# Kernel tuning notes

Hardware: AMD Instinct MI355X
Metric: run time of the kernel (lower is better)

The kernel has to match this reference:

```python
import jax, jax.numpy as jnp
import numpy as np

NUM_HEADS = 16
MAX_LEN = 2048


def setup_inputs() -> dict:
    key = jax.random.key(0)
    ks = jax.random.split(key, 10)
    L, B, C = 2048, 2, 1024
    s = 0.02
    return {
        "x": jax.random.normal(ks[0], (L, B, C), dtype=jnp.float32),
        "Wq": jax.random.normal(ks[1], (C, C), dtype=jnp.float32) * s,
        "bq": jnp.zeros((C,), dtype=jnp.float32),
        "Wk": jax.random.normal(ks[2], (C, C), dtype=jnp.float32) * s,
        "bk": jnp.zeros((C,), dtype=jnp.float32),
        "Wv": jax.random.normal(ks[3], (C, C), dtype=jnp.float32) * s,
        "bv": jnp.zeros((C,), dtype=jnp.float32),
        "Wo": jax.random.normal(ks[4], (C, C), dtype=jnp.float32) * s,
        "bo": jnp.zeros((C,), dtype=jnp.float32),
        "rel": jax.random.normal(ks[5], (2 * MAX_LEN - 1,), dtype=jnp.float32) * s,
    }


def reference(x, Wq, bq, Wk, bk, Wv, bv, Wo, bo, rel):
    L, B, C = x.shape
    H = NUM_HEADS
    hd = C // H
    scale = hd ** (-0.5)
    xb = jnp.transpose(x, (1, 0, 2))  # (B, L, C)

    def heads(y):  # (B, L, C) -> (B, H, L, hd)
        return jnp.transpose(y.reshape(B, L, H, hd), (0, 2, 1, 3))

    Q = heads(xb @ Wq + bq)
    K = heads(xb @ Wk + bk)
    V = heads(xb @ Wv + bv)

    scores = jnp.einsum("bhqd,bhkd->bhqk", Q, K)  # (B, H, L, L)
    # relative-position bias gather: offset = k - q + max_len - 1
    idx = jnp.arange(L)[None, :] - jnp.arange(L)[:, None] + (MAX_LEN - 1)
    R = rel[idx]  # (L, L)
    scores = (scores + R[None, None, :, :]) * scale
    w = jax.nn.softmax(scores, axis=-1)
    attn = jnp.einsum("bhqk,bhkd->bhqd", w, V)  # (B, H, L, hd)
    attn = jnp.transpose(attn, (0, 2, 1, 3)).reshape(B, L, C)
    attn = jnp.transpose(attn, (1, 0, 2))  # (L, B, C)
    return attn @ Wo + bo
```

## Files before the change

kernel.cpp:

```cpp
#include <hip/hip_runtime.h>

#define L_SEQ 2048
#define BATCH 2
#define CDIM  1024
#define NH    16
#define HD    64

typedef __attribute__((ext_vector_type(8))) short short8;
typedef __attribute__((ext_vector_type(4))) float floatx4;

#define QSCALE 0.18033688011112042f

__device__ __forceinline__ unsigned short f2bf(float f){
  unsigned int u = __builtin_bit_cast(unsigned int, f);
  u += 0x7fffu + ((u >> 16) & 1u);
  return (unsigned short)(u >> 16);
}

__device__ __forceinline__ void gload_lds16(const void* g, void* l){
  typedef __attribute__((address_space(1))) void gv_t;
  typedef __attribute__((address_space(3))) void sv_t;
  __builtin_amdgcn_global_load_lds((gv_t*)(void*)g, (sv_t*)l, 16, 0, 0);
}

__global__ void __launch_bounds__(256) prep_x(const float* __restrict__ x,
                                              unsigned short* __restrict__ xb){
  int idx = blockIdx.x * 256 + threadIdx.x;
  int c4 = idx & 255;
  int lb = idx >> 8;
  int b  = lb & (BATCH - 1);
  int l  = lb >> 1;
  float4 v = ((const float4*)x)[idx];
  ushort4 s;
  s.x = f2bf(v.x); s.y = f2bf(v.y); s.z = f2bf(v.z); s.w = f2bf(v.w);
  *(ushort4*)&xb[(size_t)(b*L_SEQ + l)*CDIM + c4*4] = s;
}

__global__ void __launch_bounds__(256) prep_w(const float* __restrict__ Wq,
    const float* __restrict__ Wk, const float* __restrict__ Wv,
    const float* __restrict__ Wo, unsigned short* __restrict__ Wqkvt,
    unsigned short* __restrict__ Wot){
  __shared__ float tile[32][33];
  int z = blockIdx.z;
  const float* W = (z==0)?Wq:(z==1)?Wk:(z==2)?Wv:Wo;
  unsigned short* dst = (z==3) ? Wot : (Wqkvt + (size_t)z*CDIM*CDIM);
  int tx = threadIdx.x & 31, ty = threadIdx.x >> 5;
  int X = blockIdx.x*32, Y = blockIdx.y*32;
  #pragma unroll
  for (int i=0;i<4;i++)
    tile[ty + i*8][tx] = W[(size_t)(Y + ty + i*8)*CDIM + X + tx];
  __syncthreads();
  #pragma unroll
  for (int i=0;i<4;i++)
    dst[(size_t)(X + ty + i*8)*CDIM + Y + tx] = f2bf(tile[tx][ty + i*8]);
}

template<int MODE>
__global__ void __launch_bounds__(256) gemm_bt(
    const unsigned short* __restrict__ A,
    const unsigned short* __restrict__ Bt,
    int Kdim,
    const float* __restrict__ b0, const float* __restrict__ b1,
    const float* __restrict__ b2,
    unsigned short* __restrict__ qo, unsigned short* __restrict__ ko,
    unsigned short* __restrict__ vo, float* __restrict__ out)
{
  __shared__ unsigned short Asm[128*32];
  __shared__ unsigned short Bsm[128*32];
  const int t    = threadIdx.x;
  const int lane = t & 63;
  const int wave = t >> 6;
  const int wr = wave >> 1, wc = wave & 1;
  const int g = lane >> 4, lr = lane & 15;
  const int rowA0 = blockIdx.x * 128;
  const int rowB0 = blockIdx.y * 128;

  floatx4 acc[4][4] = {};

  const int r_st = t >> 2;
  const int k_st = (t & 3) * 8;

  for (int k0 = 0; k0 < Kdim; k0 += 32) {
    const unsigned short* ga = A  + (size_t)(rowA0 + r_st) * Kdim + k0 + k_st;
    const unsigned short* gb = Bt + (size_t)(rowB0 + r_st) * Kdim + k0 + k_st;
    gload_lds16(ga,                   &Asm[t*8]);
    gload_lds16(ga + (size_t)64*Kdim, &Asm[2048 + t*8]);
    gload_lds16(gb,                   &Bsm[t*8]);
    gload_lds16(gb + (size_t)64*Kdim, &Bsm[2048 + t*8]);
    __syncthreads();
    short8 af[4], bfr[4];
    #pragma unroll
    for (int mi=0;mi<4;mi++)
      af[mi] = *(const short8*)&Asm[(wr*64 + mi*16 + lr)*32 + g*8];
    #pragma unroll
    for (int ni=0;ni<4;ni++)
      bfr[ni] = *(const short8*)&Bsm[(wc*64 + ni*16 + lr)*32 + g*8];
    #pragma unroll
    for (int mi=0;mi<4;mi++)
      #pragma unroll
      for (int ni=0;ni<4;ni++)
        acc[mi][ni] = __builtin_amdgcn_mfma_f32_16x16x32_bf16(af[mi], bfr[ni], acc[mi][ni], 0, 0, 0);
    __syncthreads();
  }

  #pragma unroll
  for (int mi=0;mi<4;mi++){
    const int rb = rowA0 + wr*64 + mi*16 + g*4;
    #pragma unroll
    for (int ni=0;ni<4;ni++){
      const int col = rowB0 + wc*64 + ni*16 + lr;
      if (MODE == 0) {
        const int sec = col >> 10;
        const int nl  = col & 1023;
        const int h = nl >> 6, d = nl & 63;
        const float* bp = (sec==0) ? b0 : (sec==1) ? b1 : b2;
        const float bias = bp[nl];
        #pragma unroll
        for (int r=0;r<4;r++){
          const int row = rb + r;
          const int b = row >> 11, l = row & 2047;
          float v = acc[mi][ni][r] + bias;
          if (sec == 0) v *= QSCALE;
          const unsigned short hv = f2bf(v);
          const size_t bh = (size_t)(b*NH + h);
          if (sec == 0)      qo[(bh*L_SEQ + l)*HD + d] = hv;
          else if (sec == 1) ko[(bh*L_SEQ + l)*HD + d] = hv;
          else               vo[(bh*HD + d)*L_SEQ + l] = hv;
        }
      } else {
        const float bias = b0[col];
        #pragma unroll
        for (int r=0;r<4;r++){
          const int row = rb + r;
          const int b = row >> 11, l = row & 2047;
          out[((size_t)l*BATCH + b)*CDIM + col] = acc[mi][ni][r] + bias;
        }
      }
    }
  }
}

__global__ void __launch_bounds__(256) attn_kernel(
    const unsigned short* __restrict__ Qb, const unsigned short* __restrict__ Kb,
    const unsigned short* __restrict__ Vt, const float* __restrict__ rel,
    unsigned short* __restrict__ Ab)
{
  __shared__ unsigned short Ks[2][64*64];
  __shared__ unsigned short Vs[2][64*64];
  __shared__ unsigned int Pl[4*16*32];
  const int bh = blockIdx.x;
  const int qb = blockIdx.y;
  const int t = threadIdx.x, lane = t & 63, wave = t >> 6;
  const int g = lane >> 4, lr = lane & 15;

  const unsigned short* Qp = Qb + (size_t)bh * (L_SEQ*HD);
  const unsigned short* Kp = Kb + (size_t)bh * (L_SEQ*HD);
  const unsigned short* Vp = Vt + (size_t)bh * (HD*L_SEQ);

  const int q0 = qb*64 + wave*16;
  const short8 qf0 = *(const short8*)&Qp[(size_t)(q0 + lr)*HD + g*8];
  const short8 qf1 = *(const short8*)&Qp[(size_t)(q0 + lr)*HD + 32 + g*8];

  const float* relp = rel + (2047 - q0 - lr + g*4);

  unsigned int* pw = Pl + wave*512 + lr*32;
  const int swz = lr & 7;

  const int srow = t >> 3;
  const int sxor = (t & 7) ^ (srow & 7);

  const unsigned short* kg = Kp + (size_t)srow*HD + sxor*8;
  const unsigned short* vg = Vp + (size_t)srow*L_SEQ + sxor*8;

  floatx4 o[4] = {};
  float m = -1e30f, lsum = 0.f;

  gload_lds16(kg,           &Ks[0][t*8]);
  gload_lds16(kg + 32*HD,   &Ks[0][2048 + t*8]);
  gload_lds16(vg,           &Vs[0][t*8]);
  gload_lds16(vg + (size_t)32*L_SEQ, &Vs[0][2048 + t*8]);
  __syncthreads();

  int cur = 0;
  for (int kb = 0; kb < L_SEQ; kb += 64) {
    {
      const int kbn = (kb + 64) & (L_SEQ - 1);
      const unsigned short* kgn = kg + (size_t)kbn*HD;
      const unsigned short* vgn = vg + kbn;
      unsigned short* kd = &Ks[cur^1][0];
      unsigned short* vd = &Vs[cur^1][0];
      gload_lds16(kgn,                    kd + t*8);
      gload_lds16(kgn + 32*HD,            kd + 2048 + t*8);
      gload_lds16(vgn,                    vd + t*8);
      gload_lds16(vgn + (size_t)32*L_SEQ, vd + 2048 + t*8);
    }

    float relv[16];
    #pragma unroll
    for (int j=0;j<4;j++)
      #pragma unroll
      for (int r=0;r<4;r++)
        relv[4*j+r] = relp[kb + 16*j + r];

    const unsigned short* kbuf = &Ks[cur][0];
    floatx4 s[4];
    #pragma unroll
    for (int j=0;j<4;j++){
      const int row = j*16 + lr;
      const short8 k0 = *(const short8*)&kbuf[row*64 + ((g    ) ^ swz)*8];
      const short8 k1 = *(const short8*)&kbuf[row*64 + ((4 + g) ^ swz)*8];
      floatx4 z = {};
      z = __builtin_amdgcn_mfma_f32_16x16x32_bf16(k0, qf0, z, 0,0,0);
      z = __builtin_amdgcn_mfma_f32_16x16x32_bf16(k1, qf1, z, 0,0,0);
      s[j] = z;
    }

    float p[16];
    #pragma unroll
    for (int j=0;j<4;j++)
      #pragma unroll
      for (int r=0;r<4;r++)
        p[4*j+r] = fmaf(relv[4*j+r], QSCALE, s[j][r]);

    float ma = fmaxf(fmaxf(fmaxf(p[0],p[1]),fmaxf(p[2],p[3])),
                     fmaxf(fmaxf(p[4],p[5]),fmaxf(p[6],p[7])));
    float mb = fmaxf(fmaxf(fmaxf(p[8],p[9]),fmaxf(p[10],p[11])),
                     fmaxf(fmaxf(p[12],p[13]),fmaxf(p[14],p[15])));
    float mx = fmaxf(ma, mb);
    mx = fmaxf(mx, __shfl_xor(mx, 16, 64));
    mx = fmaxf(mx, __shfl_xor(mx, 32, 64));
    const float mn = fmaxf(m, mx);
    const float al = exp2f(m - mn);
    m = mn;
    #pragma unroll
    for (int i=0;i<16;i++) p[i] = exp2f(p[i] - mn);
    float t0 = (p[0]+p[1]) + (p[2]+p[3]);
    float t1 = (p[4]+p[5]) + (p[6]+p[7]);
    float t2 = (p[8]+p[9]) + (p[10]+p[11]);
    float t3 = (p[12]+p[13]) + (p[14]+p[15]);
    float ss = (t0+t1) + (t2+t3);
    ss += __shfl_xor(ss, 16, 64);
    ss += __shfl_xor(ss, 32, 64);
    lsum = lsum*al + ss;
    #pragma unroll
    for (int fb=0;fb<4;fb++)
      #pragma unroll
      for (int r=0;r<4;r++) o[fb][r] *= al;

    #pragma unroll
    for (int j=0;j<4;j++){
      unsigned lo = (unsigned)f2bf(p[4*j])   | ((unsigned)f2bf(p[4*j+1])<<16);
      unsigned hi = (unsigned)f2bf(p[4*j+2]) | ((unsigned)f2bf(p[4*j+3])<<16);
      const int unit = (2*j + (g>>1)) ^ swz;
      *(uint2*)&pw[unit*4 + (g&1)*2] = make_uint2(lo, hi);
    }
    asm volatile("" ::: "memory");
    const short8 pf0 = *(const short8*)&pw[((    g) ^ swz)*4];
    const short8 pf1 = *(const short8*)&pw[((4 + g) ^ swz)*4];
    asm volatile("" ::: "memory");

    const unsigned short* vbuf = &Vs[cur][0];
    #pragma unroll
    for (int fb=0; fb<4; fb++){
      const int row = fb*16 + lr;
      const short8 v0 = *(const short8*)&vbuf[row*64 + ((g    ) ^ swz)*8];
      const short8 v1 = *(const short8*)&vbuf[row*64 + ((4 + g) ^ swz)*8];
      o[fb] = __builtin_amdgcn_mfma_f32_16x16x32_bf16(v0, pf0, o[fb], 0,0,0);
      o[fb] = __builtin_amdgcn_mfma_f32_16x16x32_bf16(v1, pf1, o[fb], 0,0,0);
    }

    __syncthreads();
    cur ^= 1;
  }

  const float inv = 1.f / lsum;
  const int b = bh >> 4, h = bh & 15;
  unsigned short* outp = &Ab[((size_t)(b*L_SEQ + q0 + lr))*CDIM + h*HD];
  #pragma unroll
  for (int fb=0; fb<4; fb++){
    #pragma unroll
    for (int rp=0; rp<2; rp++){
      const float v0 = o[fb][2*rp]   * inv;
      const float v1 = o[fb][2*rp+1] * inv;
      *(unsigned int*)&outp[fb*16 + g*4 + 2*rp] =
          (unsigned)f2bf(v0) | ((unsigned)f2bf(v1) << 16);
    }
  }
}

extern "C" void kernel_launch(void* const* d_in, const int* in_sizes, int n_in,
                              void* d_out, int out_size, void* d_ws, size_t ws_size,
                              hipStream_t stream) {
  const float* x   = (const float*)d_in[0];
  const float* Wq  = (const float*)d_in[1];
  const float* bq  = (const float*)d_in[2];
  const float* Wk  = (const float*)d_in[3];
  const float* bk  = (const float*)d_in[4];
  const float* Wv  = (const float*)d_in[5];
  const float* bv  = (const float*)d_in[6];
  const float* Wo  = (const float*)d_in[7];
  const float* bo  = (const float*)d_in[8];
  const float* rel = (const float*)d_in[9];
  float* out = (float*)d_out;

  char* ws = (char*)d_ws;
  unsigned short* Xb    = (unsigned short*)(ws);
  unsigned short* Wqkvt = (unsigned short*)(ws + (8u  << 20));
  unsigned short* Wot   = (unsigned short*)(ws + (14u << 20));
  unsigned short* Qb    = (unsigned short*)(ws + (16u << 20));
  unsigned short* Kb    = (unsigned short*)(ws + (24u << 20));
  unsigned short* Vt    = (unsigned short*)(ws + (32u << 20));
  unsigned short* Ab    = Xb;

  prep_x<<<4096, 256, 0, stream>>>(x, Xb);
  prep_w<<<dim3(32,32,4), 256, 0, stream>>>(Wq, Wk, Wv, Wo, Wqkvt, Wot);
  gemm_bt<0><<<dim3(32,24), 256, 0, stream>>>(Xb, Wqkvt, CDIM, bq, bk, bv,
                                              Qb, Kb, Vt, nullptr);
  attn_kernel<<<dim3(32,32), 256, 0, stream>>>(Qb, Kb, Vt, rel, Ab);
  gemm_bt<1><<<dim3(32,8), 256, 0, stream>>>(Ab, Wot, CDIM, bo, nullptr, nullptr,
                                             nullptr, nullptr, nullptr, out);
}
```

Baseline: 248.8 us.

## Lazy softmax rescale, packed bf16 converts, XCD-swizzled GEMM tiles, smaller output-GEMM tiles

The attention loop now skips the running-max update and the output rescale unless some lane's new max exceeds the stored max by more than 8 (log2 domain). This removes per-tile shuffles and multiplies but allows unnormalized values to grow by up to 2^8 before rescaling. Manual f32-to-bf16 rounding is replaced with the v_cvt_pk_bf16_f32 instruction. The GEMMs remap block indices so consecutive blocks are spread across the 8 XCDs. The output projection uses 64-row tiles on a 64x8 grid, giving more workgroups to fill the CUs.

```diff
diff --git a/kernel.cpp b/kernel.cpp
--- a/kernel.cpp
+++ b/kernel.cpp
@@ -15,6 +15,12 @@
   unsigned int u = __builtin_bit_cast(unsigned int, f);
   u += 0x7fffu + ((u >> 16) & 1u);
   return (unsigned short)(u >> 16);
+}
+
+__device__ __forceinline__ unsigned cvtpk(float lo, float hi){
+  unsigned r;
+  asm("v_cvt_pk_bf16_f32 %0, %1, %2" : "=v"(r) : "v"(lo), "v"(hi));
+  return r;
 }
 
 __device__ __forceinline__ void gload_lds16(const void* g, void* l){
@@ -65,17 +71,27 @@
     unsigned short* __restrict__ qo, unsigned short* __restrict__ ko,
     unsigned short* __restrict__ vo, float* __restrict__ out)
 {
-  __shared__ unsigned short Asm[128*32];
+  constexpr int BM = (MODE==0) ? 128 : 64;
+  constexpr int NF = (MODE==0) ? 4 : 2;
+  constexpr int GX = (MODE==0) ? 32 : 64;
+  constexpr int NWG = (MODE==0) ? 768 : 512;
+  constexpr int CPX = NWG/8;
+
+  __shared__ unsigned short Asm[BM*32];
   __shared__ unsigned short Bsm[128*32];
   const int t    = threadIdx.x;
   const int lane = t & 63;
   const int wave = t >> 6;
-  const int wr = wave >> 1, wc = wave & 1;
+  const int wr = (MODE==0) ? (wave >> 1) : 0;
+  const int wc = (MODE==0) ? (wave & 1)  : wave;
   const int g = lane >> 4, lr = lane & 15;
-  const int rowA0 = blockIdx.x * 128;
-  const int rowB0 = blockIdx.y * 128;
-
-  floatx4 acc[4][4] = {};
+
+  const int flat = blockIdx.y*GX + blockIdx.x;
+  const int swz  = (flat & 7)*CPX + (flat >> 3);
+  const int rowA0 = (swz % GX) * BM;
+  const int rowB0 = (swz / GX) * 128;
+
+  floatx4 acc[4][NF] = {};
 
   const int r_st = t >> 2;
   const int k_st = (t & 3) * 8;
@@ -83,22 +99,23 @@
   for (int k0 = 0; k0 < Kdim; k0 += 32) {
     const unsigned short* ga = A  + (size_t)(rowA0 + r_st) * Kdim + k0 + k_st;
     const unsigned short* gb = Bt + (size_t)(rowB0 + r_st) * Kdim + k0 + k_st;
-    gload_lds16(ga,                   &Asm[t*8]);
-    gload_lds16(ga + (size_t)64*Kdim, &Asm[2048 + t*8]);
+    gload_lds16(ga, &Asm[t*8]);
+    if constexpr (MODE==0)
+      gload_lds16(ga + (size_t)64*Kdim, &Asm[2048 + t*8]);
     gload_lds16(gb,                   &Bsm[t*8]);
     gload_lds16(gb + (size_t)64*Kdim, &Bsm[2048 + t*8]);
     __syncthreads();
-    short8 af[4], bfr[4];
+    short8 af[4], bfr[NF];
     #pragma unroll
     for (int mi=0;mi<4;mi++)
       af[mi] = *(const short8*)&Asm[(wr*64 + mi*16 + lr)*32 + g*8];
     #pragma unroll
-    for (int ni=0;ni<4;ni++)
-      bfr[ni] = *(const short8*)&Bsm[(wc*64 + ni*16 + lr)*32 + g*8];
+    for (int ni=0;ni<NF;ni++)
+      bfr[ni] = *(const short8*)&Bsm[(wc*(NF*16) + ni*16 + lr)*32 + g*8];
     #pragma unroll
     for (int mi=0;mi<4;mi++)
       #pragma unroll
-      for (int ni=0;ni<4;ni++)
+      for (int ni=0;ni<NF;ni++)
         acc[mi][ni] = __builtin_amdgcn_mfma_f32_16x16x32_bf16(af[mi], bfr[ni], acc[mi][ni], 0, 0, 0);
     __syncthreads();
   }
@@ -107,8 +124,8 @@
   for (int mi=0;mi<4;mi++){
     const int rb = rowA0 + wr*64 + mi*16 + g*4;
     #pragma unroll
-    for (int ni=0;ni<4;ni++){
-      const int col = rowB0 + wc*64 + ni*16 + lr;
+    for (int ni=0;ni<NF;ni++){
+      const int col = rowB0 + wc*(NF*16) + ni*16 + lr;
       if (MODE == 0) {
         const int sec = col >> 10;
         const int nl  = col & 1023;
@@ -226,14 +243,23 @@
                      fmaxf(fmaxf(p[4],p[5]),fmaxf(p[6],p[7])));
     float mb = fmaxf(fmaxf(fmaxf(p[8],p[9]),fmaxf(p[10],p[11])),
                      fmaxf(fmaxf(p[12],p[13]),fmaxf(p[14],p[15])));
-    float mx = fmaxf(ma, mb);
-    mx = fmaxf(mx, __shfl_xor(mx, 16, 64));
-    mx = fmaxf(mx, __shfl_xor(mx, 32, 64));
-    const float mn = fmaxf(m, mx);
-    const float al = exp2f(m - mn);
-    m = mn;
-    #pragma unroll
-    for (int i=0;i<16;i++) p[i] = exp2f(p[i] - mn);
+    float mxl = fmaxf(ma, mb);
+
+    if (!__all(mxl <= m + 8.f)) {
+      float mx = fmaxf(mxl, __shfl_xor(mxl, 16, 64));
+      mx = fmaxf(mx, __shfl_xor(mx, 32, 64));
+      const float mn = fmaxf(m, mx);
+      const float al = exp2f(m - mn);
+      m = mn;
+      lsum *= al;
+      #pragma unroll
+      for (int fb=0;fb<4;fb++)
+        #pragma unroll
+        for (int r=0;r<4;r++) o[fb][r] *= al;
+    }
+
+    #pragma unroll
+    for (int i=0;i<16;i++) p[i] = exp2f(p[i] - m);
     float t0 = (p[0]+p[1]) + (p[2]+p[3]);
     float t1 = (p[4]+p[5]) + (p[6]+p[7]);
     float t2 = (p[8]+p[9]) + (p[10]+p[11]);
@@ -241,16 +267,12 @@
     float ss = (t0+t1) + (t2+t3);
     ss += __shfl_xor(ss, 16, 64);
     ss += __shfl_xor(ss, 32, 64);
-    lsum = lsum*al + ss;
-    #pragma unroll
-    for (int fb=0;fb<4;fb++)
-      #pragma unroll
-      for (int r=0;r<4;r++) o[fb][r] *= al;
+    lsum += ss;
 
     #pragma unroll
     for (int j=0;j<4;j++){
-      unsigned lo = (unsigned)f2bf(p[4*j])   | ((unsigned)f2bf(p[4*j+1])<<16);
-      unsigned hi = (unsigned)f2bf(p[4*j+2]) | ((unsigned)f2bf(p[4*j+3])<<16);
+      unsigned lo = cvtpk(p[4*j],   p[4*j+1]);
+      unsigned hi = cvtpk(p[4*j+2], p[4*j+3]);
       const int unit = (2*j + (g>>1)) ^ swz;
       *(uint2*)&pw[unit*4 + (g&1)*2] = make_uint2(lo, hi);
     }
@@ -280,10 +302,8 @@
   for (int fb=0; fb<4; fb++){
     #pragma unroll
     for (int rp=0; rp<2; rp++){
-      const float v0 = o[fb][2*rp]   * inv;
-      const float v1 = o[fb][2*rp+1] * inv;
       *(unsigned int*)&outp[fb*16 + g*4 + 2*rp] =
-          (unsigned)f2bf(v0) | ((unsigned)f2bf(v1) << 16);
+          cvtpk(o[fb][2*rp] * inv, o[fb][2*rp+1] * inv);
     }
   }
 }
@@ -317,6 +337,6 @@
   gemm_bt<0><<<dim3(32,24), 256, 0, stream>>>(Xb, Wqkvt, CDIM, bq, bk, bv,
                                               Qb, Kb, Vt, nullptr);
   attn_kernel<<<dim3(32,32), 256, 0, stream>>>(Qb, Kb, Vt, rel, Ab);
-  gemm_bt<1><<<dim3(32,8), 256, 0, stream>>>(Ab, Wot, CDIM, bo, nullptr, nullptr,
+  gemm_bt<1><<<dim3(64,8), 256, 0, stream>>>(Ab, Wot, CDIM, bo, nullptr, nullptr,
                                              nullptr, nullptr, nullptr, out);
 }
```

Result: slower. 254.2 us (+2.2%).
